# Optimization experiments

Measured on AMD Instinct MI355X. Metric: run time of the kernel, lower is better.

The kernel has to match this reference:

```python
import jax, jax.numpy as jnp
import numpy as np

N_SUBJECTS, C_IN, C_OUT = 128, 273, 273
B, T = 256, 360


def setup_inputs() -> dict:
    key = jax.random.key(0)
    k1, k2, k3 = jax.random.split(key, 3)
    x = jax.random.normal(k1, (B, C_IN, T), dtype=jnp.float32)
    subjects = jax.random.randint(k2, (B,), 0, N_SUBJECTS, dtype=jnp.int64)
    weights = jax.random.normal(k3, (N_SUBJECTS, C_IN, C_OUT), dtype=jnp.float32)
    return {"x": x, "subjects": subjects, "weights": weights}


def reference(x, subjects, weights):
    # Gather per-sample weight matrix: (B, C, D)
    w = weights[subjects]
    # bct,bcd -> bdt : per-sample channel remap applied at every timestep
    return jnp.einsum('bct,bcd->bdt', x, w)
```

## Files before the change

### kernel.cpp

```cpp
#include <hip/hip_runtime.h>
#include <hip/hip_bf16.h>

#define NBATCH 256
#define NC 273
#define ND 273
#define NT 360

#define THREADS 512
#define BM 288
#define BN 128
#define BNV 120
#define BK 32
#define LDK 40
#define KITERS 9

typedef __bf16 bf16_t;
typedef bf16_t bf16x4 __attribute__((ext_vector_type(4)));
typedef bf16_t bf16x8 __attribute__((ext_vector_type(8)));
typedef float  f32x4  __attribute__((ext_vector_type(4)));

__global__ __launch_bounds__(THREADS, 1) void subject_gemm(
    const float* __restrict__ x,
    const int*   __restrict__ subjects,
    const float* __restrict__ w,
    float*       __restrict__ out)
{
    const int raw  = blockIdx.x;
    const int xcd  = raw & 7;
    const int slot = raw >> 3;
    const int b    = xcd * 32 + slot / 3;
    const int tt   = slot % 3;
    const int t0   = tt * BNV;
    const int s    = subjects[b];

    const float* __restrict__ xb = x + (size_t)b * NC * NT;
    const float* __restrict__ ws = w + (size_t)s * NC * ND;

    __shared__ __align__(16) bf16_t As[BM * LDK];
    __shared__ __align__(16) bf16_t Bs[BN * LDK];

    const int tid   = threadIdx.x;
    const int lane  = tid & 63;
    const int wid   = tid >> 6;
    const int wm    = wid >> 2;
    const int wn    = wid & 3;
    const int l16   = lane & 15;
    const int khalf = lane >> 4;

    int offA[5], gA[5];
#pragma unroll
    for (int j = 0; j < 5; ++j) {
        const int i  = tid + THREADS * j;
        const int ii = (i < 2304) ? i : 2303;
        const int d  = ii % BM;
        const int kq = ii / BM;
        offA[j] = d * LDK + kq * 4;
        gA[j]   = kq * 4 * ND + d;
    }
    int offB[2], gB[2];
#pragma unroll
    for (int j = 0; j < 2; ++j) {
        const int i  = tid + THREADS * j;
        const int t  = i & (BN - 1);
        const int kq = i >> 7;
        const int tc = (t < BNV) ? t : (BNV - 1);
        offB[j] = t * LDK + kq * 4;
        gB[j]   = kq * 4 * NT + t0 + tc;
    }
    const bool haveJ4 = (tid < 2304 - 4 * THREADS);

    float ra[5][4], rb[2][4];

    auto loadA_full = [&](int kk) {
        const int base = kk * ND;
#pragma unroll
        for (int j = 0; j < 4; ++j)
#pragma unroll
            for (int u = 0; u < 4; ++u)
                ra[j][u] = ws[base + gA[j] + u * ND];
        if (haveJ4)
#pragma unroll
            for (int u = 0; u < 4; ++u)
                ra[4][u] = ws[base + gA[4] + u * ND];
    };
    auto loadB_full = [&](int kk) {
        const int base = kk * NT;
#pragma unroll
        for (int j = 0; j < 2; ++j)
#pragma unroll
            for (int u = 0; u < 4; ++u)
                rb[j][u] = xb[base + gB[j] + u * NT];
    };
    auto loadA_tail = [&]() {
#pragma unroll
        for (int j = 0; j < 5; ++j) {
            if (j == 4 && !haveJ4) break;
            const int i  = tid + THREADS * j;
            const int d  = i % BM;
            const int kq = i / BM;
#pragma unroll
            for (int u = 0; u < 4; ++u) {
                const int c = 256 + kq * 4 + u;
                const bool ok = (c < NC) && (d < ND);
                ra[j][u] = ok ? ws[c * ND + d] : 0.f;
            }
        }
    };
    auto loadB_tail = [&]() {
#pragma unroll
        for (int j = 0; j < 2; ++j) {
            const int i  = tid + THREADS * j;
            const int t  = i & (BN - 1);
            const int kq = i >> 7;
            const int col = t0 + ((t < BNV) ? t : (BNV - 1));
#pragma unroll
            for (int u = 0; u < 4; ++u) {
                const int c  = 256 + kq * 4 + u;
                const int cc = (c < NC) ? c : (NC - 1);
                rb[j][u] = xb[cc * NT + col];
            }
        }
    };
    auto stage = [&]() {
#pragma unroll
        for (int j = 0; j < 4; ++j) {
            bf16x4 v;
#pragma unroll
            for (int u = 0; u < 4; ++u) v[u] = (bf16_t)ra[j][u];
            *(bf16x4*)&As[offA[j]] = v;
        }
        if (haveJ4) {
            bf16x4 v;
#pragma unroll
            for (int u = 0; u < 4; ++u) v[u] = (bf16_t)ra[4][u];
            *(bf16x4*)&As[offA[4]] = v;
        }
#pragma unroll
        for (int j = 0; j < 2; ++j) {
            bf16x4 v;
#pragma unroll
            for (int u = 0; u < 4; ++u) v[u] = (bf16_t)rb[j][u];
            *(bf16x4*)&Bs[offB[j]] = v;
        }
    };

    f32x4 acc[9][2];
#pragma unroll
    for (int m = 0; m < 9; ++m)
#pragma unroll
        for (int n = 0; n < 2; ++n)
            acc[m][n] = (f32x4){0.f, 0.f, 0.f, 0.f};

    loadA_full(0);
    loadB_full(0);

#pragma unroll
    for (int it = 0; it < KITERS; ++it) {
        stage();
        __syncthreads();

        if (it + 1 < KITERS - 1) {
            loadA_full((it + 1) * BK);
            loadB_full((it + 1) * BK);
        } else if (it + 1 == KITERS - 1) {
            loadA_tail();
            loadB_tail();
        }

        bf16x8 bfr[2];
#pragma unroll
        for (int n = 0; n < 2; ++n)
            bfr[n] = *(const bf16x8*)&Bs[(wn * 32 + n * 16 + l16) * LDK + khalf * 8];
#pragma unroll
        for (int m = 0; m < 9; ++m) {
            const bf16x8 af = *(const bf16x8*)&As[(wm * 144 + m * 16 + l16) * LDK + khalf * 8];
#pragma unroll
            for (int n = 0; n < 2; ++n)
                acc[m][n] = __builtin_amdgcn_mfma_f32_16x16x32_bf16(af, bfr[n], acc[m][n], 0, 0, 0);
        }
        __syncthreads();
    }

    float* __restrict__ ob = out + (size_t)b * ND * NT;
#pragma unroll
    for (int m = 0; m < 9; ++m) {
#pragma unroll
        for (int n = 0; n < 2; ++n) {
            const int tc = wn * 32 + n * 16 + l16;
            const int gt = t0 + tc;
#pragma unroll
            for (int rg = 0; rg < 4; ++rg) {
                const int d = wm * 144 + m * 16 + khalf * 4 + rg;
                if (d < ND && tc < BNV)
                    ob[(size_t)d * NT + gt] = acc[m][n][rg];
            }
        }
    }
}

extern "C" void kernel_launch(void* const* d_in, const int* in_sizes, int n_in,
                              void* d_out, int out_size, void* d_ws, size_t ws_size,
                              hipStream_t stream) {
    const float* x        = (const float*)d_in[0];
    const int*   subjects = (const int*)d_in[1];
    const float* w        = (const float*)d_in[2];
    float*       out      = (float*)d_out;

    const int nblocks = NBATCH * 3;
    subject_gemm<<<nblocks, THREADS, 0, stream>>>(x, subjects, w, out);
}
```

Measured before the change: 60.49 us.

## Double-buffer LDS and registers with two-stage prefetch pipeline

Doubles the shared-memory tiles and register staging buffers so global loads run two K-steps ahead and the next tile is staged into the alternate LDS buffer while MFMAs consume the current one. This removes one barrier per iteration and hides global-load latency behind compute. The launch-bounds hint changes to allow two blocks per CU, which caps register use; the doubled register buffers plus the hoisted A fragments raise register pressure and could cause spills.

```diff
diff --git a/kernel.cpp b/kernel.cpp
--- a/kernel.cpp
+++ b/kernel.cpp
@@ -19,7 +19,7 @@
 typedef bf16_t bf16x8 __attribute__((ext_vector_type(8)));
 typedef float  f32x4  __attribute__((ext_vector_type(4)));
 
-__global__ __launch_bounds__(THREADS, 1) void subject_gemm(
+__global__ __launch_bounds__(THREADS, 2) void subject_gemm(
     const float* __restrict__ x,
     const int*   __restrict__ subjects,
     const float* __restrict__ w,
@@ -36,8 +36,8 @@
     const float* __restrict__ xb = x + (size_t)b * NC * NT;
     const float* __restrict__ ws = w + (size_t)s * NC * ND;
 
-    __shared__ __align__(16) bf16_t As[BM * LDK];
-    __shared__ __align__(16) bf16_t Bs[BN * LDK];
+    __shared__ __align__(16) bf16_t As[2][BM * LDK];
+    __shared__ __align__(16) bf16_t Bs[2][BN * LDK];
 
     const int tid   = threadIdx.x;
     const int lane  = tid & 63;
@@ -69,29 +69,29 @@
     }
     const bool haveJ4 = (tid < 2304 - 4 * THREADS);
 
-    float ra[5][4], rb[2][4];
-
-    auto loadA_full = [&](int kk) {
+    float ra[2][5][4], rb[2][2][4];
+
+    auto loadA = [&](float (&r)[5][4], int kk) {
         const int base = kk * ND;
 #pragma unroll
         for (int j = 0; j < 4; ++j)
 #pragma unroll
             for (int u = 0; u < 4; ++u)
-                ra[j][u] = ws[base + gA[j] + u * ND];
+                r[j][u] = ws[base + gA[j] + u * ND];
         if (haveJ4)
 #pragma unroll
             for (int u = 0; u < 4; ++u)
-                ra[4][u] = ws[base + gA[4] + u * ND];
-    };
-    auto loadB_full = [&](int kk) {
+                r[4][u] = ws[base + gA[4] + u * ND];
+    };
+    auto loadB = [&](float (&r)[2][4], int kk) {
         const int base = kk * NT;
 #pragma unroll
         for (int j = 0; j < 2; ++j)
 #pragma unroll
             for (int u = 0; u < 4; ++u)
-                rb[j][u] = xb[base + gB[j] + u * NT];
-    };
-    auto loadA_tail = [&]() {
+                r[j][u] = xb[base + gB[j] + u * NT];
+    };
+    auto loadA_tail = [&](float (&r)[5][4]) {
 #pragma unroll
         for (int j = 0; j < 5; ++j) {
             if (j == 4 && !haveJ4) break;
@@ -102,11 +102,11 @@
             for (int u = 0; u < 4; ++u) {
                 const int c = 256 + kq * 4 + u;
                 const bool ok = (c < NC) && (d < ND);
-                ra[j][u] = ok ? ws[c * ND + d] : 0.f;
+                r[j][u] = ok ? ws[c * ND + d] : 0.f;
             }
         }
     };
-    auto loadB_tail = [&]() {
+    auto loadB_tail = [&](float (&r)[2][4]) {
 #pragma unroll
         for (int j = 0; j < 2; ++j) {
             const int i  = tid + THREADS * j;
@@ -117,30 +117,31 @@
             for (int u = 0; u < 4; ++u) {
                 const int c  = 256 + kq * 4 + u;
                 const int cc = (c < NC) ? c : (NC - 1);
-                rb[j][u] = xb[cc * NT + col];
+                r[j][u] = xb[cc * NT + col];
             }
         }
     };
-    auto stage = [&]() {
+    auto stage = [&](const float (&rA)[5][4], const float (&rB)[2][4],
+                     bf16_t* __restrict__ dA, bf16_t* __restrict__ dB) {
 #pragma unroll
         for (int j = 0; j < 4; ++j) {
             bf16x4 v;
 #pragma unroll
-            for (int u = 0; u < 4; ++u) v[u] = (bf16_t)ra[j][u];
-            *(bf16x4*)&As[offA[j]] = v;
+            for (int u = 0; u < 4; ++u) v[u] = (bf16_t)rA[j][u];
+            *(bf16x4*)&dA[offA[j]] = v;
         }
         if (haveJ4) {
             bf16x4 v;
 #pragma unroll
-            for (int u = 0; u < 4; ++u) v[u] = (bf16_t)ra[4][u];
-            *(bf16x4*)&As[offA[4]] = v;
+            for (int u = 0; u < 4; ++u) v[u] = (bf16_t)rA[4][u];
+            *(bf16x4*)&dA[offA[4]] = v;
         }
 #pragma unroll
         for (int j = 0; j < 2; ++j) {
             bf16x4 v;
 #pragma unroll
-            for (int u = 0; u < 4; ++u) v[u] = (bf16_t)rb[j][u];
-            *(bf16x4*)&Bs[offB[j]] = v;
+            for (int u = 0; u < 4; ++u) v[u] = (bf16_t)rB[j][u];
+            *(bf16x4*)&dB[offB[j]] = v;
         }
     };
 
@@ -151,33 +152,42 @@
         for (int n = 0; n < 2; ++n)
             acc[m][n] = (f32x4){0.f, 0.f, 0.f, 0.f};
 
-    loadA_full(0);
-    loadB_full(0);
+    loadA(ra[0], 0);      loadB(rb[0], 0);
+    loadA(ra[1], BK);     loadB(rb[1], BK);
+    stage(ra[0], rb[0], As[0], Bs[0]);
+    __syncthreads();
 
 #pragma unroll
     for (int it = 0; it < KITERS; ++it) {
-        stage();
-        __syncthreads();
-
-        if (it + 1 < KITERS - 1) {
-            loadA_full((it + 1) * BK);
-            loadB_full((it + 1) * BK);
-        } else if (it + 1 == KITERS - 1) {
-            loadA_tail();
-            loadB_tail();
-        }
-
-        bf16x8 bfr[2];
+        const int cur = it & 1;
+        const bf16_t* __restrict__ Ac = As[cur];
+        const bf16_t* __restrict__ Bc = Bs[cur];
+
+        bf16x8 af[9], bfr[2];
 #pragma unroll
         for (int n = 0; n < 2; ++n)
-            bfr[n] = *(const bf16x8*)&Bs[(wn * 32 + n * 16 + l16) * LDK + khalf * 8];
-#pragma unroll
-        for (int m = 0; m < 9; ++m) {
-            const bf16x8 af = *(const bf16x8*)&As[(wm * 144 + m * 16 + l16) * LDK + khalf * 8];
+            bfr[n] = *(const bf16x8*)&Bc[(wn * 32 + n * 16 + l16) * LDK + khalf * 8];
+#pragma unroll
+        for (int m = 0; m < 9; ++m)
+            af[m] = *(const bf16x8*)&Ac[(wm * 144 + m * 16 + l16) * LDK + khalf * 8];
+
+        if (it + 2 <= KITERS - 2) {
+            loadA(ra[cur], (it + 2) * BK);
+            loadB(rb[cur], (it + 2) * BK);
+        } else if (it + 2 == KITERS - 1) {
+            loadA_tail(ra[cur]);
+            loadB_tail(rb[cur]);
+        }
+
+        if (it + 1 < KITERS)
+            stage(ra[cur ^ 1], rb[cur ^ 1], As[cur ^ 1], Bs[cur ^ 1]);
+
+#pragma unroll
+        for (int m = 0; m < 9; ++m)
 #pragma unroll
             for (int n = 0; n < 2; ++n)
-                acc[m][n] = __builtin_amdgcn_mfma_f32_16x16x32_bf16(af, bfr[n], acc[m][n], 0, 0, 0);
-        }
+                acc[m][n] = __builtin_amdgcn_mfma_f32_16x16x32_bf16(af[m], bfr[n], acc[m][n], 0, 0, 0);
+
         __syncthreads();
     }
 
```

Measured after the change: 57.17 us. 5.5% less time.
